# Performance work log

Measured on AMD Instinct MI355X. Metric: run time of the kernel, lower is better.

## Reference

```python
import jax, jax.numpy as jnp
import numpy as np

V, E, H, L, B = 32000, 128, 32, 64, 32


def setup_inputs() -> dict:
    key = jax.random.key(0)
    k0, k1, k2, k3, k4, k5 = jax.random.split(key, 6)
    stdv = 1.0 / np.sqrt(H)
    we = jax.random.uniform(k0, (V, E), minval=-stdv, maxval=stdv, dtype=jnp.float32)
    we = we.at[1].set(0.0)  # pad token row zeroed, as in original
    i2h1 = jax.random.uniform(k1, (E + H, H), minval=-stdv, maxval=stdv, dtype=jnp.float32)
    i2h2 = jax.random.uniform(k2, (E + H, H), minval=-stdv, maxval=stdv, dtype=jnp.float32)
    h2o = jax.random.uniform(k3, (2 * H, V), minval=-stdv, maxval=stdv, dtype=jnp.float32)
    bias = jnp.ones((1, H), dtype=jnp.float32)  # assigned after reset_parameters -> stays ones
    hidden_init = jax.random.normal(k4, (1, H), dtype=jnp.float32)  # plain buffer, not reset
    inp = jax.random.randint(k5, (L, B), 0, V, dtype=jnp.int64)
    return {"inp": inp, "we": we, "i2h1": i2h1, "i2h2": i2h2,
            "h2o": h2o, "bias": bias, "hidden_init": hidden_init}


def reference(inp, we, i2h1, i2h2, h2o, bias, hidden_init):
    Lr, Br = inp.shape
    Hh = hidden_init.shape[1]
    emb = we[inp]                                   # [L,B,E] embedding gather
    h0 = jnp.broadcast_to(hidden_init, (Br, Hh))    # [B,H]
    b = jnp.broadcast_to(bias, (Br, Hh))            # [B,H]

    def make_step(W):
        def step(h, e):
            h_new = jnp.tanh(jnp.concatenate([e, h], axis=1) @ W + b)
            return h_new, h_new
        return step

    # forward direction: hf[i] = hidden after consuming token i
    _, hf = jax.lax.scan(make_step(i2h1), h0, emb)
    # backward direction (scan over reversed time, flip back)
    _, hb_rev = jax.lax.scan(make_step(i2h2), h0, emb[::-1])
    hb = hb_rev[::-1]                               # hb[i] = bwd hidden after token i

    # original uses hiddenf[i] (pre-token-i fwd state) and hiddenb[i+1] (post-token-(i+1) bwd state)
    hf_used = jnp.concatenate([h0[None], hf[:-1]], axis=0)   # [L,B,H]
    hb_used = jnp.concatenate([hb[1:], h0[None]], axis=0)    # [L,B,H]

    hcat = jnp.concatenate([hf_used, hb_used], axis=-1)      # [L,B,2H]
    logits = jnp.einsum('lbh,hv->lbv', hcat, h2o)            # [L,B,V]
    return jax.nn.log_softmax(logits, axis=-1)
```

## Files before the change

kernel.cpp:

```cpp
#include <hip/hip_runtime.h>
#include <hip/hip_cooperative_groups.h>

namespace cg = cooperative_groups;

#define V_SZ 32000
#define E_SZ 128
#define H_SZ 32
#define L_SZ 64
#define B_SZ 32
#define M_TOT 2048
#define K2 64
#define NVT 125
#define GRID_F 1000

typedef __bf16 bf16x8 __attribute__((ext_vector_type(8)));
typedef float f32x4 __attribute__((ext_vector_type(4)));

__device__ __forceinline__ unsigned short f2bf(float f) {
    unsigned int u = __float_as_uint(f);
    u += 0x7FFFu + ((u >> 16) & 1u);
    return (unsigned short)(u >> 16);
}

__device__ __forceinline__ void load_vfrag(
    const __bf16* __restrict__ h2oT, int vbase, int lg, int lr,
    bf16x8 vf[4][2]) {
#pragma unroll
    for (int i = 0; i < 4; ++i) {
        const __bf16* vp = h2oT + (size_t)(vbase + i * 16 + lr) * K2 + lg * 8;
        vf[i][0] = *(const bf16x8*)(vp);
        vf[i][1] = *(const bf16x8*)(vp + 32);
    }
}

__device__ __forceinline__ void load_hfrag(
    const __bf16* __restrict__ hcat, int rowbase, int lg, int lr,
    bf16x8 hf[4][2]) {
#pragma unroll
    for (int j = 0; j < 4; ++j) {
        const __bf16* hp = hcat + (size_t)(rowbase + j * 16 + lr) * K2 + lg * 8;
        hf[j][0] = *(const bf16x8*)(hp);
        hf[j][1] = *(const bf16x8*)(hp + 32);
    }
}

__device__ __forceinline__ void tile_gemm_t(
    const bf16x8 vf[4][2], const bf16x8 hf[4][2], f32x4 acc[4][4]) {
#pragma unroll
    for (int i = 0; i < 4; ++i)
#pragma unroll
        for (int j = 0; j < 4; ++j) acc[i][j] = (f32x4){0.f, 0.f, 0.f, 0.f};
#pragma unroll
    for (int i = 0; i < 4; ++i)
#pragma unroll
        for (int j = 0; j < 4; ++j) {
            acc[i][j] = __builtin_amdgcn_mfma_f32_16x16x32_bf16(vf[i][0], hf[j][0], acc[i][j], 0, 0, 0);
            acc[i][j] = __builtin_amdgcn_mfma_f32_16x16x32_bf16(vf[i][1], hf[j][1], acc[i][j], 0, 0, 0);
        }
}

template <typename EP>
__device__ __forceinline__ void sweep4(
    const __bf16* __restrict__ hcat, int y0, int lg, int lr, EP&& ep) {
    bf16x8 hfA[4][2], hfB[4][2];
    load_hfrag(hcat, y0, lg, lr, hfA);
    load_hfrag(hcat, y0 + 64, lg, lr, hfB);
    ep(hfA, y0);
    load_hfrag(hcat, y0 + 128, lg, lr, hfA);
    ep(hfB, y0 + 64);
    load_hfrag(hcat, y0 + 192, lg, lr, hfB);
    ep(hfA, y0 + 128);
    ep(hfB, y0 + 192);
}

struct EpA {
    const bf16x8 (*vf)[2];
    float* S;
    int lane;
    __device__ __forceinline__ void operator()(const bf16x8 hf[4][2], int rowbase) const {
        f32x4 acc[4][4];
        tile_gemm_t((const bf16x8(*)[2])vf, hf, acc);
        float srow[4];
#pragma unroll
        for (int j = 0; j < 4; ++j) {
            float s = 0.f;
#pragma unroll
            for (int i = 0; i < 4; ++i)
#pragma unroll
                for (int r = 0; r < 4; ++r) s += __expf(acc[i][j][r]);
            srow[j] = s;
        }
#pragma unroll
        for (int j = 0; j < 4; ++j) {
            srow[j] += __shfl_xor(srow[j], 16, 64);
            srow[j] += __shfl_xor(srow[j], 32, 64);
        }
        if (lane < 16) {
#pragma unroll
            for (int j = 0; j < 4; ++j)
                atomicAdd(&S[rowbase + j * 16 + lane], srow[j]);
        }
    }
};

struct EpB {
    const bf16x8 (*vf)[2];
    const float* S;
    float* out;
    int vbase, lg, lr;
    __device__ __forceinline__ void operator()(const bf16x8 hf[4][2], int rowbase) const {
        float lsev[4];
#pragma unroll
        for (int j = 0; j < 4; ++j)
            lsev[j] = logf(S[rowbase + j * 16 + lr]);
        f32x4 acc[4][4];
        tile_gemm_t((const bf16x8(*)[2])vf, hf, acc);
#pragma unroll
        for (int j = 0; j < 4; ++j) {
            float* rp = out + (size_t)(rowbase + j * 16 + lr) * V_SZ + vbase + lg * 4;
#pragma unroll
            for (int i = 0; i < 4; ++i) {
                f32x4 v;
                v.x = acc[i][j].x - lsev[j];
                v.y = acc[i][j].y - lsev[j];
                v.z = acc[i][j].z - lsev[j];
                v.w = acc[i][j].w - lsev[j];
                *(f32x4*)(rp + i * 16) = v;
            }
        }
    }
};

__global__ __launch_bounds__(256) void k_prep_rnn(
    const int* __restrict__ inp, const float* __restrict__ we,
    const float* __restrict__ i2h1, const float* __restrict__ i2h2,
    const float* __restrict__ h2o, const float* __restrict__ bias,
    const float* __restrict__ hinit,
    unsigned short* __restrict__ hcat_u, unsigned short* __restrict__ h2oT_u,
    float* __restrict__ S) {
    const int tid = threadIdx.x;
    const int p = blockIdx.x;
    if (p < 500) {
        if (p == 0) {
#pragma unroll
            for (int i = tid; i < M_TOT; i += 256) S[i] = 0.f;
        }
        const int v = p * 64 + (tid & 63);
        const int kg = tid >> 6;
        unsigned int* dst = (unsigned int*)(h2oT_u + (size_t)v * K2 + kg * 16);
#pragma unroll
        for (int kk = 0; kk < 16; kk += 2) {
            const int k = kg * 16 + kk;
            float a = h2o[(size_t)k * V_SZ + v];
            float b = h2o[(size_t)(k + 1) * V_SZ + v];
            dst[kk >> 1] = (unsigned int)f2bf(a) | ((unsigned int)f2bf(b) << 16);
        }
        return;
    }
    const int w2 = p - 500;
    const int dir = w2 >> 4;
    const int bpair = w2 & 15;
    const float* W = dir ? i2h2 : i2h1;
    __shared__ float Xl[L_SZ * 2 * H_SZ];
    {
        const int j = tid & 31, bb = (tid >> 5) & 1, to = tid >> 6;
        const int b = bpair * 2 + bb;
        const float bj = bias[j];
        for (int tt = 0; tt < 16; ++tt) {
            const int t = to * 16 + tt;
            const int idx = inp[t * B_SZ + b];
            const float* er = we + (size_t)idx * E_SZ;
            float acc = bj;
#pragma unroll
            for (int k0 = 0; k0 < E_SZ; k0 += 4) {
                f32x4 e4 = *(const f32x4*)(er + k0);
                acc += e4.x * W[(k0 + 0) * H_SZ + j];
                acc += e4.y * W[(k0 + 1) * H_SZ + j];
                acc += e4.z * W[(k0 + 2) * H_SZ + j];
                acc += e4.w * W[(k0 + 3) * H_SZ + j];
            }
            Xl[(t * 2 + bb) * H_SZ + j] = acc;
        }
    }
    __syncthreads();
    if (tid < 64) {
        const int lane = tid;
        const int bb = lane >> 5;
        const int b = bpair * 2 + bb;
        const int j = lane & 31;
        const int srcbase = lane & 32;
        float wh[H_SZ];
#pragma unroll
        for (int k = 0; k < H_SZ; ++k) wh[k] = W[(E_SZ + k) * H_SZ + j];
        float h = hinit[j];
        for (int step = 0; step < L_SZ; ++step) {
            const int tt = dir ? (L_SZ - 1 - step) : step;
            hcat_u[(tt * B_SZ + b) * K2 + dir * H_SZ + j] = f2bf(h);
            float a0 = Xl[(tt * 2 + bb) * H_SZ + j];
            float a1 = 0.f, a2 = 0.f, a3 = 0.f;
#pragma unroll
            for (int k = 0; k < H_SZ; k += 4) {
                a0 += __shfl(h, srcbase | k, 64) * wh[k];
                a1 += __shfl(h, srcbase | (k + 1), 64) * wh[k + 1];
                a2 += __shfl(h, srcbase | (k + 2), 64) * wh[k + 2];
                a3 += __shfl(h, srcbase | (k + 3), 64) * wh[k + 3];
            }
            float x2 = (a0 + a1) + (a2 + a3);
            float e = __expf(2.f * x2);
            h = 1.f - 2.f * __builtin_amdgcn_rcpf(e + 1.f);
        }
    }
}

__global__ __launch_bounds__(256) void k_fused(
    const unsigned short* __restrict__ hcat_u,
    const unsigned short* __restrict__ h2oT_u,
    float* __restrict__ S, float* __restrict__ out) {
    cg::grid_group gg = cg::this_grid();
    const int tid = threadIdx.x;
    const int wave = tid >> 6, lane = tid & 63;
    const int lg = lane >> 4, lr = lane & 15;
    const int xcol = blockIdx.x >> 3;
    const int y0 = (blockIdx.x & 7) * 256;
    const int vbase = xcol * 256 + wave * 64;
    const __bf16* hcat = (const __bf16*)hcat_u;
    const __bf16* h2oT = (const __bf16*)h2oT_u;

    bf16x8 vf[4][2];
    load_vfrag(h2oT, vbase, lg, lr, vf);

    EpA epa{vf, S, lane};
    sweep4(hcat, y0, lg, lr, epa);

    __threadfence();
    gg.sync();

    EpB epb{vf, S, out, vbase, lg, lr};
    sweep4(hcat, y0, lg, lr, epb);
}

__global__ __launch_bounds__(256) void k_pass_a(
    const __bf16* __restrict__ hcat, const __bf16* __restrict__ h2oT,
    float* __restrict__ S) {
    const int tid = threadIdx.x;
    const int wave = tid >> 6, lane = tid & 63;
    const int lg = lane >> 4, lr = lane & 15;
    const int y0 = blockIdx.y * 256;
    const int vbase = blockIdx.x * 256 + wave * 64;
    bf16x8 vf[4][2];
    load_vfrag(h2oT, vbase, lg, lr, vf);
    EpA epa{vf, S, lane};
    sweep4(hcat, y0, lg, lr, epa);
}

__global__ __launch_bounds__(256) void k_pass_b(
    const __bf16* __restrict__ hcat, const __bf16* __restrict__ h2oT,
    const float* __restrict__ S, float* __restrict__ out) {
    const int tid = threadIdx.x;
    const int wave = tid >> 6, lane = tid & 63;
    const int lg = lane >> 4, lr = lane & 15;
    const int y0 = blockIdx.y * 256;
    const int vbase = blockIdx.x * 256 + wave * 64;
    bf16x8 vf[4][2];
    load_vfrag(h2oT, vbase, lg, lr, vf);
    EpB epb{vf, S, out, vbase, lg, lr};
    sweep4(hcat, y0, lg, lr, epb);
}

extern "C" void kernel_launch(void* const* d_in, const int* in_sizes, int n_in,
                              void* d_out, int out_size, void* d_ws, size_t ws_size,
                              hipStream_t stream) {
    (void)in_sizes; (void)n_in; (void)out_size; (void)ws_size;
    const int*   inp   = (const int*)d_in[0];
    const float* we    = (const float*)d_in[1];
    const float* i2h1  = (const float*)d_in[2];
    const float* i2h2  = (const float*)d_in[3];
    const float* h2o   = (const float*)d_in[4];
    const float* bias  = (const float*)d_in[5];
    const float* hinit = (const float*)d_in[6];
    float* out = (float*)d_out;
    char* ws = (char*)d_ws;
    unsigned short* hcat_u = (unsigned short*)(ws);
    unsigned short* h2oT_u = (unsigned short*)(ws + 262144);
    float*          S      = (float*)(ws + 4358144);

    k_prep_rnn<<<532, 256, 0, stream>>>(inp, we, i2h1, i2h2, h2o, bias, hinit,
                                        hcat_u, h2oT_u, S);

    hipError_t e = hipErrorUnknown;
    int occ = 0;
    if (hipOccupancyMaxActiveBlocksPerMultiprocessor(&occ, k_fused, 256, 0)
            == hipSuccess && occ * 256 >= GRID_F) {
        void* args[] = {(void*)&hcat_u, (void*)&h2oT_u, (void*)&S, (void*)&out};
        e = hipLaunchCooperativeKernel((void*)k_fused, dim3(GRID_F), dim3(256),
                                       args, 0, stream);
    }
    if (e != hipSuccess) {
        k_pass_a<<<dim3(NVT, 8), 256, 0, stream>>>(
            (const __bf16*)hcat_u, (const __bf16*)h2oT_u, S);
        k_pass_b<<<dim3(NVT, 8), 256, 0, stream>>>(
            (const __bf16*)hcat_u, (const __bf16*)h2oT_u, S, out);
    }
}
```

Measured before the change: 158.5 us.

## Shrink cooperative grid to 750 blocks with uneven row tiles and lower register pressure

```diff
diff --git a/kernel.cpp b/kernel.cpp
--- a/kernel.cpp
+++ b/kernel.cpp
@@ -11,7 +11,7 @@
 #define M_TOT 2048
 #define K2 64
 #define NVT 125
-#define GRID_F 1000
+#define GRID_F 750
 
 typedef __bf16 bf16x8 __attribute__((ext_vector_type(8)));
 typedef float f32x4 __attribute__((ext_vector_type(4)));
@@ -44,33 +44,22 @@
     }
 }
 
-__device__ __forceinline__ void tile_gemm_t(
-    const bf16x8 vf[4][2], const bf16x8 hf[4][2], f32x4 acc[4][4]) {
-#pragma unroll
-    for (int i = 0; i < 4; ++i)
-#pragma unroll
-        for (int j = 0; j < 4; ++j) acc[i][j] = (f32x4){0.f, 0.f, 0.f, 0.f};
-#pragma unroll
-    for (int i = 0; i < 4; ++i)
-#pragma unroll
-        for (int j = 0; j < 4; ++j) {
-            acc[i][j] = __builtin_amdgcn_mfma_f32_16x16x32_bf16(vf[i][0], hf[j][0], acc[i][j], 0, 0, 0);
-            acc[i][j] = __builtin_amdgcn_mfma_f32_16x16x32_bf16(vf[i][1], hf[j][1], acc[i][j], 0, 0, 0);
-        }
-}
-
 template <typename EP>
-__device__ __forceinline__ void sweep4(
-    const __bf16* __restrict__ hcat, int y0, int lg, int lr, EP&& ep) {
+__device__ __forceinline__ void sweepN(
+    const __bf16* __restrict__ hcat, int y0, int ntiles, int lg, int lr,
+    EP&& ep) {
     bf16x8 hfA[4][2], hfB[4][2];
     load_hfrag(hcat, y0, lg, lr, hfA);
-    load_hfrag(hcat, y0 + 64, lg, lr, hfB);
-    ep(hfA, y0);
-    load_hfrag(hcat, y0 + 128, lg, lr, hfA);
-    ep(hfB, y0 + 64);
-    load_hfrag(hcat, y0 + 192, lg, lr, hfB);
-    ep(hfA, y0 + 128);
-    ep(hfB, y0 + 192);
+    if (ntiles > 1) load_hfrag(hcat, y0 + 64, lg, lr, hfB);
+    for (int t = 0; t < ntiles; ++t) {
+        if (t & 1) {
+            if (t + 1 < ntiles) load_hfrag(hcat, y0 + (t + 1) * 64, lg, lr, hfA);
+            ep(hfB, y0 + t * 64);
+        } else {
+            if (t + 1 < ntiles) load_hfrag(hcat, y0 + (t + 1) * 64, lg, lr, hfB);
+            ep(hfA, y0 + t * 64);
+        }
+    }
 }
 
 struct EpA {
@@ -78,27 +67,24 @@
     float* S;
     int lane;
     __device__ __forceinline__ void operator()(const bf16x8 hf[4][2], int rowbase) const {
-        f32x4 acc[4][4];
-        tile_gemm_t((const bf16x8(*)[2])vf, hf, acc);
-        float srow[4];
 #pragma unroll
         for (int j = 0; j < 4; ++j) {
+            f32x4 a[4];
+#pragma unroll
+            for (int i = 0; i < 4; ++i) {
+                a[i] = (f32x4){0.f, 0.f, 0.f, 0.f};
+                a[i] = __builtin_amdgcn_mfma_f32_16x16x32_bf16(vf[i][0], hf[j][0], a[i], 0, 0, 0);
+                a[i] = __builtin_amdgcn_mfma_f32_16x16x32_bf16(vf[i][1], hf[j][1], a[i], 0, 0, 0);
+            }
             float s = 0.f;
 #pragma unroll
             for (int i = 0; i < 4; ++i)
 #pragma unroll
-                for (int r = 0; r < 4; ++r) s += __expf(acc[i][j][r]);
-            srow[j] = s;
-        }
-#pragma unroll
-        for (int j = 0; j < 4; ++j) {
-            srow[j] += __shfl_xor(srow[j], 16, 64);
-            srow[j] += __shfl_xor(srow[j], 32, 64);
-        }
-        if (lane < 16) {
-#pragma unroll
-            for (int j = 0; j < 4; ++j)
-                atomicAdd(&S[rowbase + j * 16 + lane], srow[j]);
+                for (int r = 0; r < 4; ++r) s += __expf(a[i][r]);
+            s += __shfl_xor(s, 16, 64);
+            s += __shfl_xor(s, 32, 64);
+            if (lane < 16)
+                atomicAdd(&S[rowbase + j * 16 + lane], s);
         }
     }
 };
@@ -113,19 +99,25 @@
 #pragma unroll
         for (int j = 0; j < 4; ++j)
             lsev[j] = logf(S[rowbase + j * 16 + lr]);
-        f32x4 acc[4][4];
-        tile_gemm_t((const bf16x8(*)[2])vf, hf, acc);
-#pragma unroll
-        for (int j = 0; j < 4; ++j) {
-            float* rp = out + (size_t)(rowbase + j * 16 + lr) * V_SZ + vbase + lg * 4;
-#pragma unroll
-            for (int i = 0; i < 4; ++i) {
+#pragma unroll
+        for (int i = 0; i < 4; ++i) {
+            f32x4 a[4];
+#pragma unroll
+            for (int j = 0; j < 4; ++j) {
+                a[j] = (f32x4){0.f, 0.f, 0.f, 0.f};
+                a[j] = __builtin_amdgcn_mfma_f32_16x16x32_bf16(vf[i][0], hf[j][0], a[j], 0, 0, 0);
+                a[j] = __builtin_amdgcn_mfma_f32_16x16x32_bf16(vf[i][1], hf[j][1], a[j], 0, 0, 0);
+            }
+#pragma unroll
+            for (int j = 0; j < 4; ++j) {
+                float* rp = out + (size_t)(rowbase + j * 16 + lr) * V_SZ
+                          + vbase + lg * 4 + i * 16;
                 f32x4 v;
-                v.x = acc[i][j].x - lsev[j];
-                v.y = acc[i][j].y - lsev[j];
-                v.z = acc[i][j].z - lsev[j];
-                v.w = acc[i][j].w - lsev[j];
-                *(f32x4*)(rp + i * 16) = v;
+                v.x = a[j].x - lsev[j];
+                v.y = a[j].y - lsev[j];
+                v.z = a[j].z - lsev[j];
+                v.w = a[j].w - lsev[j];
+                *(f32x4*)rp = v;
             }
         }
     }
@@ -212,7 +204,7 @@
     }
 }
 
-__global__ __launch_bounds__(256) void k_fused(
+__global__ __launch_bounds__(256, 3) void k_fused(
     const unsigned short* __restrict__ hcat_u,
     const unsigned short* __restrict__ h2oT_u,
     float* __restrict__ S, float* __restrict__ out) {
@@ -220,8 +212,12 @@
     const int tid = threadIdx.x;
     const int wave = tid >> 6, lane = tid & 63;
     const int lg = lane >> 4, lr = lane & 15;
-    const int xcol = blockIdx.x >> 3;
-    const int y0 = (blockIdx.x & 7) * 256;
+    const int b = blockIdx.x;
+    const int xcol = b / 6;
+    const int sub = b - xcol * 6;
+    const int tstart = (sub < 2) ? sub * 6 : 12 + (sub - 2) * 5;
+    const int ntiles = (sub < 2) ? 6 : 5;
+    const int y0 = tstart * 64;
     const int vbase = xcol * 256 + wave * 64;
     const __bf16* hcat = (const __bf16*)hcat_u;
     const __bf16* h2oT = (const __bf16*)h2oT_u;
@@ -230,13 +226,13 @@
     load_vfrag(h2oT, vbase, lg, lr, vf);
 
     EpA epa{vf, S, lane};
-    sweep4(hcat, y0, lg, lr, epa);
+    sweepN(hcat, y0, ntiles, lg, lr, epa);
 
     __threadfence();
     gg.sync();
 
     EpB epb{vf, S, out, vbase, lg, lr};
-    sweep4(hcat, y0, lg, lr, epb);
+    sweepN(hcat, y0, ntiles, lg, lr, epb);
 }
 
 __global__ __launch_bounds__(256) void k_pass_a(
@@ -250,7 +246,7 @@
     bf16x8 vf[4][2];
     load_vfrag(h2oT, vbase, lg, lr, vf);
     EpA epa{vf, S, lane};
-    sweep4(hcat, y0, lg, lr, epa);
+    sweepN(hcat, y0, 4, lg, lr, epa);
 }
 
 __global__ __launch_bounds__(256) void k_pass_b(
@@ -264,7 +260,7 @@
     bf16x8 vf[4][2];
     load_vfrag(h2oT, vbase, lg, lr, vf);
     EpB epb{vf, S, out, vbase, lg, lr};
-    sweep4(hcat, y0, lg, lr, epb);
+    sweepN(hcat, y0, 4, lg, lr, epb);
 }
 
 extern "C" void kernel_launch(void* const* d_in, const int* in_sizes, int n_in,
@@ -287,14 +283,9 @@
     k_prep_rnn<<<532, 256, 0, stream>>>(inp, we, i2h1, i2h2, h2o, bias, hinit,
                                         hcat_u, h2oT_u, S);
 
-    hipError_t e = hipErrorUnknown;
-    int occ = 0;
-    if (hipOccupancyMaxActiveBlocksPerMultiprocessor(&occ, k_fused, 256, 0)
-            == hipSuccess && occ * 256 >= GRID_F) {
-        void* args[] = {(void*)&hcat_u, (void*)&h2oT_u, (void*)&S, (void*)&out};
-        e = hipLaunchCooperativeKernel((void*)k_fused, dim3(GRID_F), dim3(256),
-                                       args, 0, stream);
-    }
+    void* args[] = {(void*)&hcat_u, (void*)&h2oT_u, (void*)&S, (void*)&out};
+    hipError_t e = hipLaunchCooperativeKernel((void*)k_fused, dim3(GRID_F),
+                                              dim3(256), args, 0, stream);
     if (e != hipSuccess) {
         k_pass_a<<<dim3(NVT, 8), 256, 0, stream>>>(
             (const __bf16*)hcat_u, (const __bf16*)h2oT_u, S);
```

Measured after the change: 280.7 us. 77.1% more time.

## Shrink cooperative grid to 750 blocks with uneven row-tile split per column

Applied to the files above, without the earlier changes.

```diff
diff --git a/kernel.cpp b/kernel.cpp
--- a/kernel.cpp
+++ b/kernel.cpp
@@ -11,7 +11,7 @@
 #define M_TOT 2048
 #define K2 64
 #define NVT 125
-#define GRID_F 1000
+#define GRID_F 750
 
 typedef __bf16 bf16x8 __attribute__((ext_vector_type(8)));
 typedef float f32x4 __attribute__((ext_vector_type(4)));
@@ -57,20 +57,6 @@
             acc[i][j] = __builtin_amdgcn_mfma_f32_16x16x32_bf16(vf[i][0], hf[j][0], acc[i][j], 0, 0, 0);
             acc[i][j] = __builtin_amdgcn_mfma_f32_16x16x32_bf16(vf[i][1], hf[j][1], acc[i][j], 0, 0, 0);
         }
-}
-
-template <typename EP>
-__device__ __forceinline__ void sweep4(
-    const __bf16* __restrict__ hcat, int y0, int lg, int lr, EP&& ep) {
-    bf16x8 hfA[4][2], hfB[4][2];
-    load_hfrag(hcat, y0, lg, lr, hfA);
-    load_hfrag(hcat, y0 + 64, lg, lr, hfB);
-    ep(hfA, y0);
-    load_hfrag(hcat, y0 + 128, lg, lr, hfA);
-    ep(hfB, y0 + 64);
-    load_hfrag(hcat, y0 + 192, lg, lr, hfB);
-    ep(hfA, y0 + 128);
-    ep(hfB, y0 + 192);
 }
 
 struct EpA {
@@ -130,6 +116,17 @@
         }
     }
 };
+
+template <typename EP>
+__device__ __forceinline__ void sweepS(
+    const __bf16* __restrict__ hcat, int y0, int ntiles, int lg, int lr,
+    EP&& ep) {
+    for (int t = 0; t < ntiles; ++t) {
+        bf16x8 hf[4][2];
+        load_hfrag(hcat, y0 + t * 64, lg, lr, hf);
+        ep(hf, y0 + t * 64);
+    }
+}
 
 __global__ __launch_bounds__(256) void k_prep_rnn(
     const int* __restrict__ inp, const float* __restrict__ we,
@@ -212,7 +209,7 @@
     }
 }
 
-__global__ __launch_bounds__(256) void k_fused(
+__global__ __launch_bounds__(256, 3) void k_fused(
     const unsigned short* __restrict__ hcat_u,
     const unsigned short* __restrict__ h2oT_u,
     float* __restrict__ S, float* __restrict__ out) {
@@ -220,8 +217,12 @@
     const int tid = threadIdx.x;
     const int wave = tid >> 6, lane = tid & 63;
     const int lg = lane >> 4, lr = lane & 15;
-    const int xcol = blockIdx.x >> 3;
-    const int y0 = (blockIdx.x & 7) * 256;
+    const int b = blockIdx.x;
+    const int xcol = b / 6;
+    const int sub = b - xcol * 6;
+    const int tstart = (sub < 2) ? sub * 6 : 12 + (sub - 2) * 5;
+    const int ntiles = (sub < 2) ? 6 : 5;
+    const int y0 = tstart * 64;
     const int vbase = xcol * 256 + wave * 64;
     const __bf16* hcat = (const __bf16*)hcat_u;
     const __bf16* h2oT = (const __bf16*)h2oT_u;
@@ -230,13 +231,13 @@
     load_vfrag(h2oT, vbase, lg, lr, vf);
 
     EpA epa{vf, S, lane};
-    sweep4(hcat, y0, lg, lr, epa);
+    sweepS(hcat, y0, ntiles, lg, lr, epa);
 
     __threadfence();
     gg.sync();
 
     EpB epb{vf, S, out, vbase, lg, lr};
-    sweep4(hcat, y0, lg, lr, epb);
+    sweepS(hcat, y0, ntiles, lg, lr, epb);
 }
 
 __global__ __launch_bounds__(256) void k_pass_a(
@@ -250,7 +251,7 @@
     bf16x8 vf[4][2];
     load_vfrag(h2oT, vbase, lg, lr, vf);
     EpA epa{vf, S, lane};
-    sweep4(hcat, y0, lg, lr, epa);
+    sweepS(hcat, y0, 4, lg, lr, epa);
 }
 
 __global__ __launch_bounds__(256) void k_pass_b(
@@ -264,7 +265,7 @@
     bf16x8 vf[4][2];
     load_vfrag(h2oT, vbase, lg, lr, vf);
     EpB epb{vf, S, out, vbase, lg, lr};
-    sweep4(hcat, y0, lg, lr, epb);
+    sweepS(hcat, y0, 4, lg, lr, epb);
 }
 
 extern "C" void kernel_launch(void* const* d_in, const int* in_sizes, int n_in,
@@ -287,14 +288,9 @@
     k_prep_rnn<<<532, 256, 0, stream>>>(inp, we, i2h1, i2h2, h2o, bias, hinit,
                                         hcat_u, h2oT_u, S);
 
-    hipError_t e = hipErrorUnknown;
-    int occ = 0;
-    if (hipOccupancyMaxActiveBlocksPerMultiprocessor(&occ, k_fused, 256, 0)
-            == hipSuccess && occ * 256 >= GRID_F) {
-        void* args[] = {(void*)&hcat_u, (void*)&h2oT_u, (void*)&S, (void*)&out};
-        e = hipLaunchCooperativeKernel((void*)k_fused, dim3(GRID_F), dim3(256),
-                                       args, 0, stream);
-    }
+    void* args[] = {(void*)&hcat_u, (void*)&h2oT_u, (void*)&S, (void*)&out};
+    hipError_t e = hipLaunchCooperativeKernel((void*)k_fused, dim3(GRID_F),
+                                              dim3(256), args, 0, stream);
     if (e != hipSuccess) {
         k_pass_a<<<dim3(NVT, 8), 256, 0, stream>>>(
             (const __bf16*)hcat_u, (const __bf16*)h2oT_u, S);
```

Result: slower. 272.5 us (+71.9%).
